# Performance work log

Measured on AMD Instinct MI355X. Metric: run time of the kernel, lower is better.

## Reference

```python
import jax, jax.numpy as jnp
import numpy as np

EMBED_DIM = 256
NUM_HEADS = 8
HEAD_DIM = EMBED_DIM // NUM_HEADS
CPB_HIDDEN = 64


def setup_inputs() -> dict:
    key = jax.random.key(0)
    ks = jax.random.split(key, 12)
    B, Q, K = 4, 900, 1024
    s = 0.02
    return {
        "nodes": jax.random.normal(ks[0], (B, Q, EMBED_DIM), jnp.float32),
        "images_data": jax.random.normal(ks[1], (B, K, EMBED_DIM), jnp.float32),
        "images_mask": jnp.zeros((B, K), dtype=bool),
        "relative_distances": jax.random.normal(ks[2], (B, Q, K, 2), jnp.float32),
        "Wq": jax.random.normal(ks[3], (EMBED_DIM, EMBED_DIM), jnp.float32) * s,
        "bq": jnp.zeros((EMBED_DIM,), jnp.float32),
        "Wkv": jax.random.normal(ks[4], (2 * EMBED_DIM, EMBED_DIM), jnp.float32) * s,
        "bkv": jnp.zeros((2 * EMBED_DIM,), jnp.float32),
        "Wc1": jax.random.normal(ks[5], (CPB_HIDDEN, 2), jnp.float32) * 0.5,
        "bc1": jnp.zeros((CPB_HIDDEN,), jnp.float32),
        "Wc2": jax.random.normal(ks[6], (NUM_HEADS, CPB_HIDDEN), jnp.float32) * 0.1,
        "bc2": jnp.zeros((NUM_HEADS,), jnp.float32),
        "Wo": jax.random.normal(ks[7], (EMBED_DIM, EMBED_DIM), jnp.float32) * s,
        "bo": jnp.zeros((EMBED_DIM,), jnp.float32),
    }


def reference(nodes, images_data, images_mask, relative_distances,
              Wq, bq, Wkv, bkv, Wc1, bc1, Wc2, bc2, Wo, bo):
    B, Q, K, _ = relative_distances.shape
    H, D = NUM_HEADS, HEAD_DIM

    # query / key / value projections
    q = nodes @ Wq.T + bq                       # [B, Q, E]
    q = q.reshape(B, Q, H, D).transpose(0, 2, 1, 3)  # [B, H, Q, D]
    kv = images_data @ Wkv.T + bkv              # [B, K, 2E]
    kv = kv.reshape(B, K, 2, H, D).transpose(2, 0, 3, 1, 4)  # [2, B, H, K, D]
    k, v = kv[0], kv[1]

    # continuous position bias MLP: [B,Q,K,2] -> [B,Q,K,H]
    h = jax.nn.relu(relative_distances @ Wc1.T + bc1)
    cpb = h @ Wc2.T + bc2                       # [B, Q, K, H]
    cpb = cpb.transpose(0, 3, 1, 2)             # [B, H, Q, K]

    # mask out padded image positions
    att_mask = jnp.where(images_mask[:, None, None, :], -jnp.inf, cpb)

    # scaled dot-product attention with additive mask
    scale = 1.0 / jnp.sqrt(jnp.asarray(D, q.dtype))
    scores = jnp.einsum("bhqd,bhkd->bhqk", q, k) * scale + att_mask
    attn = jax.nn.softmax(scores, axis=-1)
    out = jnp.einsum("bhqk,bhkd->bhqd", attn, v)  # [B, H, Q, D]

    out = out.transpose(0, 2, 1, 3).reshape(B, Q, H * D)
    return out @ Wo.T + bo
```

## Files before the change

### kernel.cpp

```cpp
#include <hip/hip_runtime.h>
#include <hip/hip_bf16.h>

typedef float f32x4 __attribute__((ext_vector_type(4)));
typedef short short8 __attribute__((ext_vector_type(8)));

static __device__ __forceinline__ short f2bf(float x) {
  union { __hip_bfloat16 b; short s; } u;
  u.b = __float2bfloat16(x);
  return u.s;
}
static __device__ __forceinline__ float bf2f(short s) {
  union { unsigned u; float f; } x;
  x.u = ((unsigned)(unsigned short)s) << 16;
  return x.f;
}

__global__ __launch_bounds__(256)
void cvt_bf16(const float* __restrict__ nodes, const float* __restrict__ images,
              const float* __restrict__ Wq, const float* __restrict__ Wkv,
              const float* __restrict__ Wo,
              short* __restrict__ nb, short* __restrict__ ib,
              short* __restrict__ wqb, short* __restrict__ wkvb,
              short* __restrict__ wob) {
  const int idx = blockIdx.x * 256 + threadIdx.x;
  const float* src; short* dst; int o;
  if      (idx < 115200) { src = nodes;  dst = nb;   o = idx; }
  else if (idx < 246272) { src = images; dst = ib;   o = idx - 115200; }
  else if (idx < 254464) { src = Wq;     dst = wqb;  o = idx - 246272; }
  else if (idx < 270848) { src = Wkv;    dst = wkvb; o = idx - 254464; }
  else                   { src = Wo;     dst = wob;  o = idx - 270848; }
  const float4 a = ((const float4*)src)[o * 2];
  const float4 b = ((const float4*)src)[o * 2 + 1];
  short8 v;
  v[0] = f2bf(a.x); v[1] = f2bf(a.y); v[2] = f2bf(a.z); v[3] = f2bf(a.w);
  v[4] = f2bf(b.x); v[5] = f2bf(b.y); v[6] = f2bf(b.z); v[7] = f2bf(b.w);
  *(short8*)&dst[o * 8] = v;
}

__global__ __launch_bounds__(256, 4)
void gemm_qkv_mfma(const short* __restrict__ nb, const short* __restrict__ wqb,
                   const float* __restrict__ bq, short* __restrict__ qb,
                   const short* __restrict__ ib, const short* __restrict__ wkvb,
                   const float* __restrict__ bkv, short* __restrict__ kb,
                   short* __restrict__ vT) {
  const int t = threadIdx.x, w = t >> 6, lane = t & 63;
  const int fr = lane & 15, fk = lane >> 4;
  int bid = blockIdx.x;
  const short *A, *W; const float* bias; int M, m0, n0, kvmode;
  if (bid < 228) {
    A = nb; W = wqb; bias = bq; M = 3600; kvmode = 0;
    m0 = (bid >> 2) * 64; n0 = (bid & 3) * 64;
  } else {
    bid -= 228;
    A = ib; W = wkvb; bias = bkv; M = 4096; kvmode = 1;
    m0 = (bid >> 3) * 64; n0 = (bid & 7) * 64;
  }
  int arow = m0 + w * 16 + fr; if (arow > M - 1) arow = M - 1;
  f32x4 acc[4];
  #pragma unroll
  for (int s = 0; s < 4; ++s) acc[s] = (f32x4){0.f, 0.f, 0.f, 0.f};
  #pragma unroll 2
  for (int k0 = 0; k0 < 256; k0 += 32) {
    const short8 af = *(const short8*)&A[(size_t)arow * 256 + k0 + fk * 8];
    #pragma unroll
    for (int s = 0; s < 4; ++s) {
      const short8 wf =
          *(const short8*)&W[(size_t)(n0 + s * 16 + fr) * 256 + k0 + fk * 8];
      acc[s] = __builtin_amdgcn_mfma_f32_16x16x32_bf16(af, wf, acc[s], 0, 0, 0);
    }
  }
  #pragma unroll
  for (int s = 0; s < 4; ++s)
    #pragma unroll
    for (int r = 0; r < 4; ++r) {
      const int m = m0 + w * 16 + fk * 4 + r;
      const int n = n0 + s * 16 + fr;
      const float val = acc[s][r] + bias[n];
      if (kvmode == 0) {
        if (m < 3600) qb[(size_t)m * 256 + n] = f2bf(val);
      } else {
        if (n < 256)
          kb[(size_t)m * 256 + n] = f2bf(val);
        else
          vT[((size_t)(m >> 10) * 256 + (n - 256)) * 1024 + (m & 1023)] =
              f2bf(val);
      }
    }
}

template <int NS>
__global__ __launch_bounds__(256, 4)
void gemm_out_combine(const float* __restrict__ Opart,
                      const float* __restrict__ msplit,
                      const float* __restrict__ lsplit,
                      const short* __restrict__ wob, const float* __restrict__ bo,
                      float* __restrict__ out) {
  const int t = threadIdx.x, w = t >> 6, lane = t & 63;
  const int fr = lane & 15, fk = lane >> 4;
  const int m0 = (blockIdx.x >> 2) * 64, n0 = (blockIdx.x & 3) * 64;
  int arow = m0 + w * 16 + fr; if (arow > 3599) arow = 3599;
  const int b = arow / 900, q = arow - b * 900;
  const int row912 = b * 912 + q;
  f32x4 acc[4];
  #pragma unroll
  for (int s = 0; s < 4; ++s) acc[s] = (f32x4){0.f, 0.f, 0.f, 0.f};
  #pragma unroll 2
  for (int k0 = 0; k0 < 256; k0 += 32) {
    const int h = k0 >> 5;
    float mv[NS], M = -1e30f;
    #pragma unroll
    for (int s = 0; s < NS; ++s) {
      mv[s] = msplit[((s * 4 + b) * 8 + h) * 912 + q];
      M = fmaxf(M, mv[s]);
    }
    float L = 0.f, wgt[NS];
    #pragma unroll
    for (int s = 0; s < NS; ++s) {
      wgt[s] = __expf(mv[s] - M);
      L = fmaf(lsplit[((s * 4 + b) * 8 + h) * 912 + q], wgt[s], L);
    }
    const float rL = 1.f / L;
    float av[8];
    #pragma unroll
    for (int j = 0; j < 8; ++j) av[j] = 0.f;
    #pragma unroll
    for (int s = 0; s < NS; ++s) {
      const float* op = &Opart[((size_t)s * 3648 + row912) * 256 + k0 + fk * 8];
      const float4 o0 = *(const float4*)op;
      const float4 o1 = *(const float4*)(op + 4);
      const float ws = wgt[s] * rL;
      av[0] = fmaf(o0.x, ws, av[0]); av[1] = fmaf(o0.y, ws, av[1]);
      av[2] = fmaf(o0.z, ws, av[2]); av[3] = fmaf(o0.w, ws, av[3]);
      av[4] = fmaf(o1.x, ws, av[4]); av[5] = fmaf(o1.y, ws, av[5]);
      av[6] = fmaf(o1.z, ws, av[6]); av[7] = fmaf(o1.w, ws, av[7]);
    }
    short8 af;
    #pragma unroll
    for (int j = 0; j < 8; ++j) af[j] = f2bf(av[j]);
    #pragma unroll
    for (int s = 0; s < 4; ++s) {
      const short8 wf =
          *(const short8*)&wob[(size_t)(n0 + s * 16 + fr) * 256 + k0 + fk * 8];
      acc[s] = __builtin_amdgcn_mfma_f32_16x16x32_bf16(af, wf, acc[s], 0, 0, 0);
    }
  }
  #pragma unroll
  for (int s = 0; s < 4; ++s)
    #pragma unroll
    for (int r = 0; r < 4; ++r) {
      const int m = m0 + w * 16 + fk * 4 + r;
      const int n = n0 + s * 16 + fr;
      if (m < 3600) out[(size_t)m * 256 + n] = acc[s][r] + bo[n];
    }
}

#define SCALE 0.17677669529663687f

#define BAR()                                              \
  asm volatile("s_waitcnt lgkmcnt(0)" ::: "memory");       \
  __builtin_amdgcn_s_barrier();                            \
  asm volatile("" ::: "memory")

template <int KLEN>
__global__ __launch_bounds__(512, 2)
void attn_part(const __hip_bfloat16* __restrict__ qb,
               const __hip_bfloat16* __restrict__ kb,
               const __hip_bfloat16* __restrict__ vT,
               const float* __restrict__ dist,
               const unsigned char* __restrict__ mask,
               const float* __restrict__ Wc1, const float* __restrict__ bc1,
               const float* __restrict__ Wc2, const float* __restrict__ bc2,
               float* __restrict__ Opart,
               float* __restrict__ msplit,
               float* __restrict__ lsplit) {
  constexpr int NCH = KLEN / 32;
  __shared__ short cpb_s[2][8 * 552];
  __shared__ short ps_s[8][640];

  const int t    = threadIdx.x;
  const int b    = blockIdx.x / 57;
  const int q0   = (blockIdx.x % 57) * 16;
  const int sp   = blockIdx.y;
  const int kb0  = sp * KLEN;
  const int w    = t >> 6;
  const int lane = t & 63;
  const int fr   = lane & 15;
  const int fk   = lane >> 4;

  float w1x[2][8], w1y[2][8], w1b[2][8];
  #pragma unroll
  for (int m = 0; m < 2; ++m)
    #pragma unroll
    for (int jj = 0; jj < 8; ++jj) {
      const int j = m * 32 + fk * 8 + jj;
      w1x[m][jj] = Wc1[2 * j];
      w1y[m][jj] = Wc1[2 * j + 1];
      w1b[m][jj] = bc1[j];
    }
  short8 w2f[2];
  #pragma unroll
  for (int m = 0; m < 2; ++m)
    #pragma unroll
    for (int jj = 0; jj < 8; ++jj) {
      const float v = (fr < 8) ? Wc2[fr * 64 + m * 32 + fk * 8 + jj] : 0.f;
      w2f[m][jj] = f2bf(v);
    }
  const float b2add = (fr < 8) ? bc2[fr] : 0.f;

  int qrow = q0 + fr; if (qrow > 899) qrow = 899;
  const short8 aq = *(const short8*)&qb[(size_t)(b * 900 + qrow) * 256 +
                                        w * 32 + fk * 8];

  const float* dptr[4];
  float2 d2cur[4];
  #pragma unroll
  for (int t4 = 0; t4 < 4; ++t4) {
    int qg = q0 + 2 * w + (t4 >> 1); if (qg > 899) qg = 899;
    dptr[t4] = dist +
        ((size_t)(b * 900 + qg) * 1024 + kb0 + (t4 & 1) * 16 + fr) * 2;
    d2cur[t4] = *(const float2*)dptr[t4];
  }

  f32x4 of[2];
  of[0] = (f32x4){0.f, 0.f, 0.f, 0.f};
  of[1] = (f32x4){0.f, 0.f, 0.f, 0.f};
  float mreg[4], lreg[4];
  #pragma unroll
  for (int r = 0; r < 4; ++r) { mreg[r] = -1e30f; lreg[r] = 0.f; }

  for (int c = 0; c < NCH; ++c) {
    const int k0 = kb0 + c * 32;
    const int cn = (c < NCH - 1) ? c + 1 : c;
    short* cpb_c = cpb_s[c & 1];

    float2 d2n[4];
    #pragma unroll
    for (int t4 = 0; t4 < 4; ++t4)
      d2n[t4] = *(const float2*)(dptr[t4] + (size_t)cn * 64);
    const short8 kf0 = *(const short8*)
        &kb[(size_t)(b * 1024 + k0 + fr) * 256 + w * 32 + fk * 8];
    const short8 kf1 = *(const short8*)
        &kb[(size_t)(b * 1024 + k0 + 16 + fr) * 256 + w * 32 + fk * 8];
    const short8 bv0 = *(const short8*)
        &vT[(size_t)(b * 256 + w * 32 + fr) * 1024 + k0 + fk * 8];
    const short8 bv1 = *(const short8*)
        &vT[(size_t)(b * 256 + w * 32 + 16 + fr) * 1024 + k0 + fk * 8];
    const bool mk0 = mask[b * 1024 + k0 + fr] != 0;
    const bool mk1 = mask[b * 1024 + k0 + 16 + fr] != 0;

    #pragma unroll
    for (int t4 = 0; t4 < 4; ++t4) {
      const float dx = d2cur[t4].x, dy = d2cur[t4].y;
      short8 a0, a1;
      #pragma unroll
      for (int jj = 0; jj < 8; ++jj) {
        const float h0 =
            fmaxf(fmaf(w1x[0][jj], dx, fmaf(w1y[0][jj], dy, w1b[0][jj])), 0.f);
        const float h1 =
            fmaxf(fmaf(w1x[1][jj], dx, fmaf(w1y[1][jj], dy, w1b[1][jj])), 0.f);
        a0[jj] = f2bf(h0);
        a1[jj] = f2bf(h1);
      }
      f32x4 z = {0.f, 0.f, 0.f, 0.f};
      f32x4 dcp = __builtin_amdgcn_mfma_f32_16x16x32_bf16(a1, w2f[1], z, 0, 0, 0);
      dcp = __builtin_amdgcn_mfma_f32_16x16x32_bf16(a0, w2f[0], dcp, 0, 0, 0);
      const int qloc = 2 * w + (t4 >> 1);
      const int kbase = (t4 & 1) * 16;
      if (fr < 8) {
        #pragma unroll
        for (int rr = 0; rr < 4; ++rr)
          cpb_c[fr * 552 + qloc * 34 + kbase + fk * 4 + rr] =
              f2bf(dcp[rr] + b2add);
      }
      __builtin_amdgcn_sched_barrier(0);
    }

    BAR();

    f32x4 z = {0.f, 0.f, 0.f, 0.f};
    __builtin_amdgcn_s_setprio(1);
    const f32x4 sc0 = __builtin_amdgcn_mfma_f32_16x16x32_bf16(aq, kf0, z, 0, 0, 0);
    const f32x4 sc1 = __builtin_amdgcn_mfma_f32_16x16x32_bf16(aq, kf1, z, 0, 0, 0);
    __builtin_amdgcn_s_setprio(0);

    float s0v[4], s1v[4];
    bool need = false;
    #pragma unroll
    for (int r = 0; r < 4; ++r) {
      const int q = fk * 4 + r;
      const float cv0 = bf2f(cpb_c[w * 552 + q * 34 + fr]);
      const float cv1 = bf2f(cpb_c[w * 552 + q * 34 + 16 + fr]);
      s0v[r] = mk0 ? -1e30f : fmaf(sc0[r], SCALE, cv0);
      s1v[r] = mk1 ? -1e30f : fmaf(sc1[r], SCALE, cv1);
      need = need || (fmaxf(s0v[r], s1v[r]) > mreg[r] + 8.f);
    }
    if (__any((int)need)) {
      #pragma unroll
      for (int r = 0; r < 4; ++r) {
        float mx = fmaxf(s0v[r], s1v[r]);
        mx = fmaxf(mx, __shfl_xor(mx, 1));
        mx = fmaxf(mx, __shfl_xor(mx, 2));
        mx = fmaxf(mx, __shfl_xor(mx, 4));
        mx = fmaxf(mx, __shfl_xor(mx, 8));
        const float mnew = fmaxf(mreg[r], mx);
        const float al = __expf(mreg[r] - mnew);
        of[0][r] *= al;
        of[1][r] *= al;
        lreg[r] *= al;
        mreg[r] = mnew;
      }
    }
    #pragma unroll
    for (int r = 0; r < 4; ++r) {
      const int q = fk * 4 + r;
      const float p0 = __expf(s0v[r] - mreg[r]);
      const float p1 = __expf(s1v[r] - mreg[r]);
      ps_s[w][q * 40 + fr]      = f2bf(p0);
      ps_s[w][q * 40 + 16 + fr] = f2bf(p1);
      lreg[r] += p0 + p1;
    }

    asm volatile("s_waitcnt lgkmcnt(0)" ::: "memory");
    __builtin_amdgcn_sched_barrier(0);

    const short8 ap = *(const short8*)&ps_s[w][fr * 40 + fk * 8];
    __builtin_amdgcn_s_setprio(1);
    of[0] = __builtin_amdgcn_mfma_f32_16x16x32_bf16(ap, bv0, of[0], 0, 0, 0);
    of[1] = __builtin_amdgcn_mfma_f32_16x16x32_bf16(ap, bv1, of[1], 0, 0, 0);
    __builtin_amdgcn_s_setprio(0);

    #pragma unroll
    for (int t4 = 0; t4 < 4; ++t4) d2cur[t4] = d2n[t4];
  }

  #pragma unroll
  for (int r = 0; r < 4; ++r) {
    lreg[r] += __shfl_xor(lreg[r], 1);
    lreg[r] += __shfl_xor(lreg[r], 2);
    lreg[r] += __shfl_xor(lreg[r], 4);
    lreg[r] += __shfl_xor(lreg[r], 8);
  }

  #pragma unroll
  for (int s = 0; s < 2; ++s)
    #pragma unroll
    for (int r = 0; r < 4; ++r) {
      const int qg = q0 + fk * 4 + r;
      Opart[((size_t)sp * 3648 + b * 912 + qg) * 256 + w * 32 + s * 16 + fr] =
          of[s][r];
    }
  if (fr == 0) {
    #pragma unroll
    for (int r = 0; r < 4; ++r) {
      const int qg = q0 + fk * 4 + r;
      msplit[((sp * 4 + b) * 8 + w) * 912 + qg] = mreg[r];
      lsplit[((sp * 4 + b) * 8 + w) * 912 + qg] = lreg[r];
    }
  }
}

extern "C" void kernel_launch(void* const* d_in, const int* in_sizes, int n_in,
                              void* d_out, int out_size, void* d_ws, size_t ws_size,
                              hipStream_t stream) {
  const float* nodes  = (const float*)d_in[0];
  const float* images = (const float*)d_in[1];
  const unsigned char* mask = (const unsigned char*)d_in[2];
  const float* dist   = (const float*)d_in[3];
  const float* Wq     = (const float*)d_in[4];
  const float* bq     = (const float*)d_in[5];
  const float* Wkv    = (const float*)d_in[6];
  const float* bkv    = (const float*)d_in[7];
  const float* Wc1    = (const float*)d_in[8];
  const float* bc1    = (const float*)d_in[9];
  const float* Wc2    = (const float*)d_in[10];
  const float* bc2    = (const float*)d_in[11];
  const float* Wo     = (const float*)d_in[12];
  const float* bo     = (const float*)d_in[13];
  float* out = (float*)d_out;

  char* wp = (char*)d_ws;
  short* qb = (short*)wp;
  short* kb = (short*)(wp + 1843200);
  short* vT = (short*)(wp + 3940352);
  char*  S  = wp + 6037504;
  short* nb   = (short*)S;
  short* ib   = (short*)(S + 1843200);
  short* wqb  = (short*)(S + 3940352);
  short* wkvb = (short*)(S + 4071424);
  float* Opart = (float*)S;

  const size_t opart_b  = (size_t)3648 * 256 * 4;
  const size_t ml_b     = (size_t)4 * 8 * 912 * 4;
  const size_t need4 = 6037504u + 4 * (opart_b + 2 * ml_b) + 131072u;
  const size_t need2 = 6037504u + 2 * (opart_b + 2 * ml_b) + 131072u;
  int nsplit = 1;
  if (ws_size >= need4) nsplit = 4;
  else if (ws_size >= need2) nsplit = 2;
  const size_t Ssize = (nsplit == 4) ? 4 * (opart_b + 2 * ml_b)
                     : (nsplit == 2) ? 2 * (opart_b + 2 * ml_b)
                                     : 4333568u;
  short* wob = (short*)(S + ((Ssize > 4333568u) ? Ssize : 4333568u));
  float* msplit = Opart + (size_t)nsplit * 3648 * 256;
  float* lsplit = msplit + (size_t)nsplit * 4 * 8 * 912;

  cvt_bf16<<<1090, 256, 0, stream>>>(nodes, images, Wq, Wkv, Wo,
                                     nb, ib, wqb, wkvb, wob);
  gemm_qkv_mfma<<<740, 256, 0, stream>>>(nb, wqb, bq, qb, ib, wkvb, bkv, kb, vT);

  if (nsplit == 4) {
    attn_part<256><<<dim3(228, 4), 512, 0, stream>>>(
        (const __hip_bfloat16*)qb, (const __hip_bfloat16*)kb,
        (const __hip_bfloat16*)vT, dist, mask, Wc1, bc1, Wc2, bc2,
        Opart, msplit, lsplit);
    gemm_out_combine<4><<<228, 256, 0, stream>>>(Opart, msplit, lsplit,
                                                 wob, bo, out);
  } else if (nsplit == 2) {
    attn_part<512><<<dim3(228, 2), 512, 0, stream>>>(
        (const __hip_bfloat16*)qb, (const __hip_bfloat16*)kb,
        (const __hip_bfloat16*)vT, dist, mask, Wc1, bc1, Wc2, bc2,
        Opart, msplit, lsplit);
    gemm_out_combine<2><<<228, 256, 0, stream>>>(Opart, msplit, lsplit,
                                                 wob, bo, out);
  } else {
    attn_part<1024><<<dim3(228, 1), 512, 0, stream>>>(
        (const __hip_bfloat16*)qb, (const __hip_bfloat16*)kb,
        (const __hip_bfloat16*)vT, dist, mask, Wc1, bc1, Wc2, bc2,
        Opart, msplit, lsplit);
    gemm_out_combine<1><<<228, 256, 0, stream>>>(Opart, msplit, lsplit,
                                                 wob, bo, out);
  }
}
```

Measured before the change: 133.6 us.

## Split CPB MLP into a separate kernel and stream bias into barrier-free attention

The position-bias MLP moves out of the attention kernel into a standalone kernel that writes a bf16 bias tensor [B,H,Q,K] to workspace. A new attention kernel reads that bias from global memory, drops the shared-memory CPB buffer and block barrier, and prefetches K, V, bias and mask one chunk ahead in registers. It uses 2 K-splits instead of 4. The trade is about 60 MB of extra global traffic (bias write plus read) and one more launch, in exchange for removing the barrier and the MLP compute from the attention loop. The path only runs when the workspace is large enough.

```diff
diff --git a/kernel.cpp b/kernel.cpp
--- a/kernel.cpp
+++ b/kernel.cpp
@@ -3,6 +3,7 @@
 
 typedef float f32x4 __attribute__((ext_vector_type(4)));
 typedef short short8 __attribute__((ext_vector_type(8)));
+typedef short short4v __attribute__((ext_vector_type(4)));
 
 static __device__ __forceinline__ short f2bf(float x) {
   union { __hip_bfloat16 b; short s; } u;
@@ -88,6 +89,455 @@
     }
 }
 
+__global__ __launch_bounds__(512, 2)
+void cpb_mlp(const float* __restrict__ dist,
+             const float* __restrict__ Wc1, const float* __restrict__ bc1,
+             const float* __restrict__ Wc2, const float* __restrict__ bc2,
+             short* __restrict__ cpbg) {
+  const int t = threadIdx.x;
+  const int b = blockIdx.x / 57;
+  const int q0 = (blockIdx.x % 57) * 16;
+  const int kb0 = blockIdx.y * 256;
+  const int w = t >> 6, lane = t & 63;
+  const int fr = lane & 15, fk = lane >> 4;
+
+  float w1x[2][8], w1y[2][8], w1b[2][8];
+  #pragma unroll
+  for (int m = 0; m < 2; ++m)
+    #pragma unroll
+    for (int jj = 0; jj < 8; ++jj) {
+      const int j = m * 32 + fk * 8 + jj;
+      w1x[m][jj] = Wc1[2 * j];
+      w1y[m][jj] = Wc1[2 * j + 1];
+      w1b[m][jj] = bc1[j];
+    }
+  short8 w2f[2];
+  #pragma unroll
+  for (int m = 0; m < 2; ++m)
+    #pragma unroll
+    for (int jj = 0; jj < 8; ++jj) {
+      const float v = (fr < 8) ? Wc2[fr * 64 + m * 32 + fk * 8 + jj] : 0.f;
+      w2f[m][jj] = f2bf(v);
+    }
+  const float b2add = (fr < 8) ? bc2[fr] : 0.f;
+
+  const float* dptr[4];
+  float2 d2cur[4];
+  #pragma unroll
+  for (int t4 = 0; t4 < 4; ++t4) {
+    int qg = q0 + 2 * w + (t4 >> 1); if (qg > 899) qg = 899;
+    dptr[t4] = dist +
+        ((size_t)(b * 900 + qg) * 1024 + kb0 + (t4 & 1) * 16 + fr) * 2;
+    d2cur[t4] = *(const float2*)dptr[t4];
+  }
+
+  for (int c = 0; c < 8; ++c) {
+    const int k0 = kb0 + c * 32;
+    const int cn = (c < 7) ? c + 1 : c;
+    float2 d2n[4];
+    #pragma unroll
+    for (int t4 = 0; t4 < 4; ++t4)
+      d2n[t4] = *(const float2*)(dptr[t4] + (size_t)cn * 64);
+
+    #pragma unroll
+    for (int t4 = 0; t4 < 4; ++t4) {
+      const float dx = d2cur[t4].x, dy = d2cur[t4].y;
+      short8 a0, a1;
+      #pragma unroll
+      for (int jj = 0; jj < 8; ++jj) {
+        const float h0 =
+            fmaxf(fmaf(w1x[0][jj], dx, fmaf(w1y[0][jj], dy, w1b[0][jj])), 0.f);
+        const float h1 =
+            fmaxf(fmaf(w1x[1][jj], dx, fmaf(w1y[1][jj], dy, w1b[1][jj])), 0.f);
+        a0[jj] = f2bf(h0);
+        a1[jj] = f2bf(h1);
+      }
+      f32x4 z = {0.f, 0.f, 0.f, 0.f};
+      f32x4 dcp = __builtin_amdgcn_mfma_f32_16x16x32_bf16(a1, w2f[1], z, 0, 0, 0);
+      dcp = __builtin_amdgcn_mfma_f32_16x16x32_bf16(a0, w2f[0], dcp, 0, 0, 0);
+      const int qloc = 2 * w + (t4 >> 1);
+      const int kbase = (t4 & 1) * 16;
+      if (fr < 8) {
+        short4v sv;
+        sv[0] = f2bf(dcp[0] + b2add); sv[1] = f2bf(dcp[1] + b2add);
+        sv[2] = f2bf(dcp[2] + b2add); sv[3] = f2bf(dcp[3] + b2add);
+        *(short4v*)&cpbg[((size_t)(b * 8 + fr) * 912 + q0 + qloc) * 1024 +
+                         k0 + kbase + fk * 4] = sv;
+      }
+      __builtin_amdgcn_sched_barrier(0);
+    }
+    #pragma unroll
+    for (int t4 = 0; t4 < 4; ++t4) d2cur[t4] = d2n[t4];
+  }
+}
+
+#define SCALE 0.17677669529663687f
+
+template <int KLEN>
+__global__ __launch_bounds__(512, 2)
+void attn_nb(const __hip_bfloat16* __restrict__ qb,
+             const __hip_bfloat16* __restrict__ kb,
+             const __hip_bfloat16* __restrict__ vT,
+             const short* __restrict__ cpbg,
+             const unsigned char* __restrict__ mask,
+             float* __restrict__ Opart,
+             float* __restrict__ msplit,
+             float* __restrict__ lsplit) {
+  constexpr int NCH = KLEN / 32;
+  __shared__ short ps_s[8][640];
+
+  const int t    = threadIdx.x;
+  const int b    = blockIdx.x / 57;
+  const int q0   = (blockIdx.x % 57) * 16;
+  const int sp   = blockIdx.y;
+  const int kb0  = sp * KLEN;
+  const int w    = t >> 6;
+  const int lane = t & 63;
+  const int fr   = lane & 15;
+  const int fk   = lane >> 4;
+
+  int qrow = q0 + fr; if (qrow > 899) qrow = 899;
+  const short8 aq = *(const short8*)&qb[(size_t)(b * 900 + qrow) * 256 +
+                                        w * 32 + fk * 8];
+
+  const short* cpbrow[4];
+  #pragma unroll
+  for (int r = 0; r < 4; ++r)
+    cpbrow[r] = cpbg + ((size_t)(b * 8 + w) * 912 + q0 + fk * 4 + r) * 1024 + fr;
+
+  f32x4 of[2];
+  of[0] = (f32x4){0.f, 0.f, 0.f, 0.f};
+  of[1] = (f32x4){0.f, 0.f, 0.f, 0.f};
+  float mreg[4], lreg[4];
+  #pragma unroll
+  for (int r = 0; r < 4; ++r) { mreg[r] = -1e30f; lreg[r] = 0.f; }
+
+  short8 kf0 = *(const short8*)
+      &kb[(size_t)(b * 1024 + kb0 + fr) * 256 + w * 32 + fk * 8];
+  short8 kf1 = *(const short8*)
+      &kb[(size_t)(b * 1024 + kb0 + 16 + fr) * 256 + w * 32 + fk * 8];
+  short8 bv0 = *(const short8*)
+      &vT[(size_t)(b * 256 + w * 32 + fr) * 1024 + kb0 + fk * 8];
+  short8 bv1 = *(const short8*)
+      &vT[(size_t)(b * 256 + w * 32 + 16 + fr) * 1024 + kb0 + fk * 8];
+  float cv0c[4], cv1c[4];
+  #pragma unroll
+  for (int r = 0; r < 4; ++r) {
+    cv0c[r] = bf2f(cpbrow[r][kb0]);
+    cv1c[r] = bf2f(cpbrow[r][kb0 + 16]);
+  }
+  bool mk0 = mask[b * 1024 + kb0 + fr] != 0;
+  bool mk1 = mask[b * 1024 + kb0 + 16 + fr] != 0;
+
+  for (int c = 0; c < NCH; ++c) {
+    const int k0 = kb0 + c * 32;
+
+    short8 kf0n = kf0, kf1n = kf1, bv0n = bv0, bv1n = bv1;
+    float cv0n[4], cv1n[4];
+    bool mk0n = mk0, mk1n = mk1;
+    if (c + 1 < NCH) {
+      const int k1 = k0 + 32;
+      kf0n = *(const short8*)
+          &kb[(size_t)(b * 1024 + k1 + fr) * 256 + w * 32 + fk * 8];
+      kf1n = *(const short8*)
+          &kb[(size_t)(b * 1024 + k1 + 16 + fr) * 256 + w * 32 + fk * 8];
+      bv0n = *(const short8*)
+          &vT[(size_t)(b * 256 + w * 32 + fr) * 1024 + k1 + fk * 8];
+      bv1n = *(const short8*)
+          &vT[(size_t)(b * 256 + w * 32 + 16 + fr) * 1024 + k1 + fk * 8];
+      #pragma unroll
+      for (int r = 0; r < 4; ++r) {
+        cv0n[r] = bf2f(cpbrow[r][k1]);
+        cv1n[r] = bf2f(cpbrow[r][k1 + 16]);
+      }
+      mk0n = mask[b * 1024 + k1 + fr] != 0;
+      mk1n = mask[b * 1024 + k1 + 16 + fr] != 0;
+    } else {
+      #pragma unroll
+      for (int r = 0; r < 4; ++r) { cv0n[r] = cv0c[r]; cv1n[r] = cv1c[r]; }
+    }
+
+    f32x4 z = {0.f, 0.f, 0.f, 0.f};
+    __builtin_amdgcn_s_setprio(1);
+    const f32x4 sc0 = __builtin_amdgcn_mfma_f32_16x16x32_bf16(aq, kf0, z, 0, 0, 0);
+    const f32x4 sc1 = __builtin_amdgcn_mfma_f32_16x16x32_bf16(aq, kf1, z, 0, 0, 0);
+    __builtin_amdgcn_s_setprio(0);
+
+    float s0v[4], s1v[4];
+    bool need = false;
+    #pragma unroll
+    for (int r = 0; r < 4; ++r) {
+      s0v[r] = mk0 ? -1e30f : fmaf(sc0[r], SCALE, cv0c[r]);
+      s1v[r] = mk1 ? -1e30f : fmaf(sc1[r], SCALE, cv1c[r]);
+      need = need || (fmaxf(s0v[r], s1v[r]) > mreg[r] + 8.f);
+    }
+    if (__any((int)need)) {
+      #pragma unroll
+      for (int r = 0; r < 4; ++r) {
+        float mx = fmaxf(s0v[r], s1v[r]);
+        mx = fmaxf(mx, __shfl_xor(mx, 1));
+        mx = fmaxf(mx, __shfl_xor(mx, 2));
+        mx = fmaxf(mx, __shfl_xor(mx, 4));
+        mx = fmaxf(mx, __shfl_xor(mx, 8));
+        const float mnew = fmaxf(mreg[r], mx);
+        const float al = __expf(mreg[r] - mnew);
+        of[0][r] *= al;
+        of[1][r] *= al;
+        lreg[r] *= al;
+        mreg[r] = mnew;
+      }
+    }
+    #pragma unroll
+    for (int r = 0; r < 4; ++r) {
+      const int q = fk * 4 + r;
+      const float p0 = __expf(s0v[r] - mreg[r]);
+      const float p1 = __expf(s1v[r] - mreg[r]);
+      ps_s[w][q * 40 + fr]      = f2bf(p0);
+      ps_s[w][q * 40 + 16 + fr] = f2bf(p1);
+      lreg[r] += p0 + p1;
+    }
+
+    asm volatile("s_waitcnt lgkmcnt(0)" ::: "memory");
+    __builtin_amdgcn_sched_barrier(0);
+
+    const short8 ap = *(const short8*)&ps_s[w][fr * 40 + fk * 8];
+    __builtin_amdgcn_s_setprio(1);
+    of[0] = __builtin_amdgcn_mfma_f32_16x16x32_bf16(ap, bv0, of[0], 0, 0, 0);
+    of[1] = __builtin_amdgcn_mfma_f32_16x16x32_bf16(ap, bv1, of[1], 0, 0, 0);
+    __builtin_amdgcn_s_setprio(0);
+
+    kf0 = kf0n; kf1 = kf1n; bv0 = bv0n; bv1 = bv1n;
+    mk0 = mk0n; mk1 = mk1n;
+    #pragma unroll
+    for (int r = 0; r < 4; ++r) { cv0c[r] = cv0n[r]; cv1c[r] = cv1n[r]; }
+  }
+
+  #pragma unroll
+  for (int r = 0; r < 4; ++r) {
+    lreg[r] += __shfl_xor(lreg[r], 1);
+    lreg[r] += __shfl_xor(lreg[r], 2);
+    lreg[r] += __shfl_xor(lreg[r], 4);
+    lreg[r] += __shfl_xor(lreg[r], 8);
+  }
+  #pragma unroll
+  for (int s = 0; s < 2; ++s)
+    #pragma unroll
+    for (int r = 0; r < 4; ++r) {
+      const int qg = q0 + fk * 4 + r;
+      Opart[((size_t)sp * 3648 + b * 912 + qg) * 256 + w * 32 + s * 16 + fr] =
+          of[s][r];
+    }
+  if (fr == 0) {
+    #pragma unroll
+    for (int r = 0; r < 4; ++r) {
+      const int qg = q0 + fk * 4 + r;
+      msplit[((sp * 4 + b) * 8 + w) * 912 + qg] = mreg[r];
+      lsplit[((sp * 4 + b) * 8 + w) * 912 + qg] = lreg[r];
+    }
+  }
+}
+
+#define BAR()                                              \
+  asm volatile("s_waitcnt lgkmcnt(0)" ::: "memory");       \
+  __builtin_amdgcn_s_barrier();                            \
+  asm volatile("" ::: "memory")
+
+template <int KLEN>
+__global__ __launch_bounds__(512, 2)
+void attn_part(const __hip_bfloat16* __restrict__ qb,
+               const __hip_bfloat16* __restrict__ kb,
+               const __hip_bfloat16* __restrict__ vT,
+               const float* __restrict__ dist,
+               const unsigned char* __restrict__ mask,
+               const float* __restrict__ Wc1, const float* __restrict__ bc1,
+               const float* __restrict__ Wc2, const float* __restrict__ bc2,
+               float* __restrict__ Opart, float* __restrict__ msplit,
+               float* __restrict__ lsplit) {
+  constexpr int NCH = KLEN / 32;
+  __shared__ short cpb_s[2][8 * 552];
+  __shared__ short ps_s[8][640];
+
+  const int t    = threadIdx.x;
+  const int b    = blockIdx.x / 57;
+  const int q0   = (blockIdx.x % 57) * 16;
+  const int sp   = blockIdx.y;
+  const int kb0  = sp * KLEN;
+  const int w    = t >> 6;
+  const int lane = t & 63;
+  const int fr   = lane & 15;
+  const int fk   = lane >> 4;
+
+  float w1x[2][8], w1y[2][8], w1b[2][8];
+  #pragma unroll
+  for (int m = 0; m < 2; ++m)
+    #pragma unroll
+    for (int jj = 0; jj < 8; ++jj) {
+      const int j = m * 32 + fk * 8 + jj;
+      w1x[m][jj] = Wc1[2 * j];
+      w1y[m][jj] = Wc1[2 * j + 1];
+      w1b[m][jj] = bc1[j];
+    }
+  short8 w2f[2];
+  #pragma unroll
+  for (int m = 0; m < 2; ++m)
+    #pragma unroll
+    for (int jj = 0; jj < 8; ++jj) {
+      const float v = (fr < 8) ? Wc2[fr * 64 + m * 32 + fk * 8 + jj] : 0.f;
+      w2f[m][jj] = f2bf(v);
+    }
+  const float b2add = (fr < 8) ? bc2[fr] : 0.f;
+
+  int qrow = q0 + fr; if (qrow > 899) qrow = 899;
+  const short8 aq = *(const short8*)&qb[(size_t)(b * 900 + qrow) * 256 +
+                                        w * 32 + fk * 8];
+
+  const float* dptr[4];
+  float2 d2cur[4];
+  #pragma unroll
+  for (int t4 = 0; t4 < 4; ++t4) {
+    int qg = q0 + 2 * w + (t4 >> 1); if (qg > 899) qg = 899;
+    dptr[t4] = dist +
+        ((size_t)(b * 900 + qg) * 1024 + kb0 + (t4 & 1) * 16 + fr) * 2;
+    d2cur[t4] = *(const float2*)dptr[t4];
+  }
+
+  f32x4 of[2];
+  of[0] = (f32x4){0.f, 0.f, 0.f, 0.f};
+  of[1] = (f32x4){0.f, 0.f, 0.f, 0.f};
+  float mreg[4], lreg[4];
+  #pragma unroll
+  for (int r = 0; r < 4; ++r) { mreg[r] = -1e30f; lreg[r] = 0.f; }
+
+  for (int c = 0; c < NCH; ++c) {
+    const int k0 = kb0 + c * 32;
+    const int cn = (c < NCH - 1) ? c + 1 : c;
+    short* cpb_c = cpb_s[c & 1];
+
+    float2 d2n[4];
+    #pragma unroll
+    for (int t4 = 0; t4 < 4; ++t4)
+      d2n[t4] = *(const float2*)(dptr[t4] + (size_t)cn * 64);
+    const short8 kf0 = *(const short8*)
+        &kb[(size_t)(b * 1024 + k0 + fr) * 256 + w * 32 + fk * 8];
+    const short8 kf1 = *(const short8*)
+        &kb[(size_t)(b * 1024 + k0 + 16 + fr) * 256 + w * 32 + fk * 8];
+    const short8 bv0 = *(const short8*)
+        &vT[(size_t)(b * 256 + w * 32 + fr) * 1024 + k0 + fk * 8];
+    const short8 bv1 = *(const short8*)
+        &vT[(size_t)(b * 256 + w * 32 + 16 + fr) * 1024 + k0 + fk * 8];
+    const bool mk0 = mask[b * 1024 + k0 + fr] != 0;
+    const bool mk1 = mask[b * 1024 + k0 + 16 + fr] != 0;
+
+    #pragma unroll
+    for (int t4 = 0; t4 < 4; ++t4) {
+      const float dx = d2cur[t4].x, dy = d2cur[t4].y;
+      short8 a0, a1;
+      #pragma unroll
+      for (int jj = 0; jj < 8; ++jj) {
+        const float h0 =
+            fmaxf(fmaf(w1x[0][jj], dx, fmaf(w1y[0][jj], dy, w1b[0][jj])), 0.f);
+        const float h1 =
+            fmaxf(fmaf(w1x[1][jj], dx, fmaf(w1y[1][jj], dy, w1b[1][jj])), 0.f);
+        a0[jj] = f2bf(h0);
+        a1[jj] = f2bf(h1);
+      }
+      f32x4 z = {0.f, 0.f, 0.f, 0.f};
+      f32x4 dcp = __builtin_amdgcn_mfma_f32_16x16x32_bf16(a1, w2f[1], z, 0, 0, 0);
+      dcp = __builtin_amdgcn_mfma_f32_16x16x32_bf16(a0, w2f[0], dcp, 0, 0, 0);
+      const int qloc = 2 * w + (t4 >> 1);
+      const int kbase = (t4 & 1) * 16;
+      if (fr < 8) {
+        #pragma unroll
+        for (int rr = 0; rr < 4; ++rr)
+          cpb_c[fr * 552 + qloc * 34 + kbase + fk * 4 + rr] =
+              f2bf(dcp[rr] + b2add);
+      }
+      __builtin_amdgcn_sched_barrier(0);
+    }
+
+    BAR();
+
+    f32x4 z = {0.f, 0.f, 0.f, 0.f};
+    __builtin_amdgcn_s_setprio(1);
+    const f32x4 sc0 = __builtin_amdgcn_mfma_f32_16x16x32_bf16(aq, kf0, z, 0, 0, 0);
+    const f32x4 sc1 = __builtin_amdgcn_mfma_f32_16x16x32_bf16(aq, kf1, z, 0, 0, 0);
+    __builtin_amdgcn_s_setprio(0);
+
+    float s0v[4], s1v[4];
+    bool need = false;
+    #pragma unroll
+    for (int r = 0; r < 4; ++r) {
+      const int q = fk * 4 + r;
+      const float cv0 = bf2f(cpb_c[w * 552 + q * 34 + fr]);
+      const float cv1 = bf2f(cpb_c[w * 552 + q * 34 + 16 + fr]);
+      s0v[r] = mk0 ? -1e30f : fmaf(sc0[r], SCALE, cv0);
+      s1v[r] = mk1 ? -1e30f : fmaf(sc1[r], SCALE, cv1);
+      need = need || (fmaxf(s0v[r], s1v[r]) > mreg[r] + 8.f);
+    }
+    if (__any((int)need)) {
+      #pragma unroll
+      for (int r = 0; r < 4; ++r) {
+        float mx = fmaxf(s0v[r], s1v[r]);
+        mx = fmaxf(mx, __shfl_xor(mx, 1));
+        mx = fmaxf(mx, __shfl_xor(mx, 2));
+        mx = fmaxf(mx, __shfl_xor(mx, 4));
+        mx = fmaxf(mx, __shfl_xor(mx, 8));
+        const float mnew = fmaxf(mreg[r], mx);
+        const float al = __expf(mreg[r] - mnew);
+        of[0][r] *= al;
+        of[1][r] *= al;
+        lreg[r] *= al;
+        mreg[r] = mnew;
+      }
+    }
+    #pragma unroll
+    for (int r = 0; r < 4; ++r) {
+      const int q = fk * 4 + r;
+      const float p0 = __expf(s0v[r] - mreg[r]);
+      const float p1 = __expf(s1v[r] - mreg[r]);
+      ps_s[w][q * 40 + fr]      = f2bf(p0);
+      ps_s[w][q * 40 + 16 + fr] = f2bf(p1);
+      lreg[r] += p0 + p1;
+    }
+
+    asm volatile("s_waitcnt lgkmcnt(0)" ::: "memory");
+    __builtin_amdgcn_sched_barrier(0);
+
+    const short8 ap = *(const short8*)&ps_s[w][fr * 40 + fk * 8];
+    __builtin_amdgcn_s_setprio(1);
+    of[0] = __builtin_amdgcn_mfma_f32_16x16x32_bf16(ap, bv0, of[0], 0, 0, 0);
+    of[1] = __builtin_amdgcn_mfma_f32_16x16x32_bf16(ap, bv1, of[1], 0, 0, 0);
+    __builtin_amdgcn_s_setprio(0);
+
+    #pragma unroll
+    for (int t4 = 0; t4 < 4; ++t4) d2cur[t4] = d2n[t4];
+  }
+
+  #pragma unroll
+  for (int r = 0; r < 4; ++r) {
+    lreg[r] += __shfl_xor(lreg[r], 1);
+    lreg[r] += __shfl_xor(lreg[r], 2);
+    lreg[r] += __shfl_xor(lreg[r], 4);
+    lreg[r] += __shfl_xor(lreg[r], 8);
+  }
+  #pragma unroll
+  for (int s = 0; s < 2; ++s)
+    #pragma unroll
+    for (int r = 0; r < 4; ++r) {
+      const int qg = q0 + fk * 4 + r;
+      Opart[((size_t)sp * 3648 + b * 912 + qg) * 256 + w * 32 + s * 16 + fr] =
+          of[s][r];
+    }
+  if (fr == 0) {
+    #pragma unroll
+    for (int r = 0; r < 4; ++r) {
+      const int qg = q0 + fk * 4 + r;
+      msplit[((sp * 4 + b) * 8 + w) * 912 + qg] = mreg[r];
+      lsplit[((sp * 4 + b) * 8 + w) * 912 + qg] = lreg[r];
+    }
+  }
+}
+
 template <int NS>
 __global__ __launch_bounds__(256, 4)
 void gemm_out_combine(const float* __restrict__ Opart,
@@ -152,211 +602,6 @@
       const int n = n0 + s * 16 + fr;
       if (m < 3600) out[(size_t)m * 256 + n] = acc[s][r] + bo[n];
     }
-}
-
-#define SCALE 0.17677669529663687f
-
-#define BAR()                                              \
-  asm volatile("s_waitcnt lgkmcnt(0)" ::: "memory");       \
-  __builtin_amdgcn_s_barrier();                            \
-  asm volatile("" ::: "memory")
-
-template <int KLEN>
-__global__ __launch_bounds__(512, 2)
-void attn_part(const __hip_bfloat16* __restrict__ qb,
-               const __hip_bfloat16* __restrict__ kb,
-               const __hip_bfloat16* __restrict__ vT,
-               const float* __restrict__ dist,
-               const unsigned char* __restrict__ mask,
-               const float* __restrict__ Wc1, const float* __restrict__ bc1,
-               const float* __restrict__ Wc2, const float* __restrict__ bc2,
-               float* __restrict__ Opart,
-               float* __restrict__ msplit,
-               float* __restrict__ lsplit) {
-  constexpr int NCH = KLEN / 32;
-  __shared__ short cpb_s[2][8 * 552];
-  __shared__ short ps_s[8][640];
-
-  const int t    = threadIdx.x;
-  const int b    = blockIdx.x / 57;
-  const int q0   = (blockIdx.x % 57) * 16;
-  const int sp   = blockIdx.y;
-  const int kb0  = sp * KLEN;
-  const int w    = t >> 6;
-  const int lane = t & 63;
-  const int fr   = lane & 15;
-  const int fk   = lane >> 4;
-
-  float w1x[2][8], w1y[2][8], w1b[2][8];
-  #pragma unroll
-  for (int m = 0; m < 2; ++m)
-    #pragma unroll
-    for (int jj = 0; jj < 8; ++jj) {
-      const int j = m * 32 + fk * 8 + jj;
-      w1x[m][jj] = Wc1[2 * j];
-      w1y[m][jj] = Wc1[2 * j + 1];
-      w1b[m][jj] = bc1[j];
-    }
-  short8 w2f[2];
-  #pragma unroll
-  for (int m = 0; m < 2; ++m)
-    #pragma unroll
-    for (int jj = 0; jj < 8; ++jj) {
-      const float v = (fr < 8) ? Wc2[fr * 64 + m * 32 + fk * 8 + jj] : 0.f;
-      w2f[m][jj] = f2bf(v);
-    }
-  const float b2add = (fr < 8) ? bc2[fr] : 0.f;
-
-  int qrow = q0 + fr; if (qrow > 899) qrow = 899;
-  const short8 aq = *(const short8*)&qb[(size_t)(b * 900 + qrow) * 256 +
-                                        w * 32 + fk * 8];
-
-  const float* dptr[4];
-  float2 d2cur[4];
-  #pragma unroll
-  for (int t4 = 0; t4 < 4; ++t4) {
-    int qg = q0 + 2 * w + (t4 >> 1); if (qg > 899) qg = 899;
-    dptr[t4] = dist +
-        ((size_t)(b * 900 + qg) * 1024 + kb0 + (t4 & 1) * 16 + fr) * 2;
-    d2cur[t4] = *(const float2*)dptr[t4];
-  }
-
-  f32x4 of[2];
-  of[0] = (f32x4){0.f, 0.f, 0.f, 0.f};
-  of[1] = (f32x4){0.f, 0.f, 0.f, 0.f};
-  float mreg[4], lreg[4];
-  #pragma unroll
-  for (int r = 0; r < 4; ++r) { mreg[r] = -1e30f; lreg[r] = 0.f; }
-
-  for (int c = 0; c < NCH; ++c) {
-    const int k0 = kb0 + c * 32;
-    const int cn = (c < NCH - 1) ? c + 1 : c;
-    short* cpb_c = cpb_s[c & 1];
-
-    float2 d2n[4];
-    #pragma unroll
-    for (int t4 = 0; t4 < 4; ++t4)
-      d2n[t4] = *(const float2*)(dptr[t4] + (size_t)cn * 64);
-    const short8 kf0 = *(const short8*)
-        &kb[(size_t)(b * 1024 + k0 + fr) * 256 + w * 32 + fk * 8];
-    const short8 kf1 = *(const short8*)
-        &kb[(size_t)(b * 1024 + k0 + 16 + fr) * 256 + w * 32 + fk * 8];
-    const short8 bv0 = *(const short8*)
-        &vT[(size_t)(b * 256 + w * 32 + fr) * 1024 + k0 + fk * 8];
-    const short8 bv1 = *(const short8*)
-        &vT[(size_t)(b * 256 + w * 32 + 16 + fr) * 1024 + k0 + fk * 8];
-    const bool mk0 = mask[b * 1024 + k0 + fr] != 0;
-    const bool mk1 = mask[b * 1024 + k0 + 16 + fr] != 0;
-
-    #pragma unroll
-    for (int t4 = 0; t4 < 4; ++t4) {
-      const float dx = d2cur[t4].x, dy = d2cur[t4].y;
-      short8 a0, a1;
-      #pragma unroll
-      for (int jj = 0; jj < 8; ++jj) {
-        const float h0 =
-            fmaxf(fmaf(w1x[0][jj], dx, fmaf(w1y[0][jj], dy, w1b[0][jj])), 0.f);
-        const float h1 =
-            fmaxf(fmaf(w1x[1][jj], dx, fmaf(w1y[1][jj], dy, w1b[1][jj])), 0.f);
-        a0[jj] = f2bf(h0);
-        a1[jj] = f2bf(h1);
-      }
-      f32x4 z = {0.f, 0.f, 0.f, 0.f};
-      f32x4 dcp = __builtin_amdgcn_mfma_f32_16x16x32_bf16(a1, w2f[1], z, 0, 0, 0);
-      dcp = __builtin_amdgcn_mfma_f32_16x16x32_bf16(a0, w2f[0], dcp, 0, 0, 0);
-      const int qloc = 2 * w + (t4 >> 1);
-      const int kbase = (t4 & 1) * 16;
-      if (fr < 8) {
-        #pragma unroll
-        for (int rr = 0; rr < 4; ++rr)
-          cpb_c[fr * 552 + qloc * 34 + kbase + fk * 4 + rr] =
-              f2bf(dcp[rr] + b2add);
-      }
-      __builtin_amdgcn_sched_barrier(0);
-    }
-
-    BAR();
-
-    f32x4 z = {0.f, 0.f, 0.f, 0.f};
-    __builtin_amdgcn_s_setprio(1);
-    const f32x4 sc0 = __builtin_amdgcn_mfma_f32_16x16x32_bf16(aq, kf0, z, 0, 0, 0);
-    const f32x4 sc1 = __builtin_amdgcn_mfma_f32_16x16x32_bf16(aq, kf1, z, 0, 0, 0);
-    __builtin_amdgcn_s_setprio(0);
-
-    float s0v[4], s1v[4];
-    bool need = false;
-    #pragma unroll
-    for (int r = 0; r < 4; ++r) {
-      const int q = fk * 4 + r;
-      const float cv0 = bf2f(cpb_c[w * 552 + q * 34 + fr]);
-      const float cv1 = bf2f(cpb_c[w * 552 + q * 34 + 16 + fr]);
-      s0v[r] = mk0 ? -1e30f : fmaf(sc0[r], SCALE, cv0);
-      s1v[r] = mk1 ? -1e30f : fmaf(sc1[r], SCALE, cv1);
-      need = need || (fmaxf(s0v[r], s1v[r]) > mreg[r] + 8.f);
-    }
-    if (__any((int)need)) {
-      #pragma unroll
-      for (int r = 0; r < 4; ++r) {
-        float mx = fmaxf(s0v[r], s1v[r]);
-        mx = fmaxf(mx, __shfl_xor(mx, 1));
-        mx = fmaxf(mx, __shfl_xor(mx, 2));
-        mx = fmaxf(mx, __shfl_xor(mx, 4));
-        mx = fmaxf(mx, __shfl_xor(mx, 8));
-        const float mnew = fmaxf(mreg[r], mx);
-        const float al = __expf(mreg[r] - mnew);
-        of[0][r] *= al;
-        of[1][r] *= al;
-        lreg[r] *= al;
-        mreg[r] = mnew;
-      }
-    }
-    #pragma unroll
-    for (int r = 0; r < 4; ++r) {
-      const int q = fk * 4 + r;
-      const float p0 = __expf(s0v[r] - mreg[r]);
-      const float p1 = __expf(s1v[r] - mreg[r]);
-      ps_s[w][q * 40 + fr]      = f2bf(p0);
-      ps_s[w][q * 40 + 16 + fr] = f2bf(p1);
-      lreg[r] += p0 + p1;
-    }
-
-    asm volatile("s_waitcnt lgkmcnt(0)" ::: "memory");
-    __builtin_amdgcn_sched_barrier(0);
-
-    const short8 ap = *(const short8*)&ps_s[w][fr * 40 + fk * 8];
-    __builtin_amdgcn_s_setprio(1);
-    of[0] = __builtin_amdgcn_mfma_f32_16x16x32_bf16(ap, bv0, of[0], 0, 0, 0);
-    of[1] = __builtin_amdgcn_mfma_f32_16x16x32_bf16(ap, bv1, of[1], 0, 0, 0);
-    __builtin_amdgcn_s_setprio(0);
-
-    #pragma unroll
-    for (int t4 = 0; t4 < 4; ++t4) d2cur[t4] = d2n[t4];
-  }
-
-  #pragma unroll
-  for (int r = 0; r < 4; ++r) {
-    lreg[r] += __shfl_xor(lreg[r], 1);
-    lreg[r] += __shfl_xor(lreg[r], 2);
-    lreg[r] += __shfl_xor(lreg[r], 4);
-    lreg[r] += __shfl_xor(lreg[r], 8);
-  }
-
-  #pragma unroll
-  for (int s = 0; s < 2; ++s)
-    #pragma unroll
-    for (int r = 0; r < 4; ++r) {
-      const int qg = q0 + fk * 4 + r;
-      Opart[((size_t)sp * 3648 + b * 912 + qg) * 256 + w * 32 + s * 16 + fr] =
-          of[s][r];
-    }
-  if (fr == 0) {
-    #pragma unroll
-    for (int r = 0; r < 4; ++r) {
-      const int qg = q0 + fk * 4 + r;
-      msplit[((sp * 4 + b) * 8 + w) * 912 + qg] = mreg[r];
-      lsplit[((sp * 4 + b) * 8 + w) * 912 + qg] = lreg[r];
-    }
-  }
 }
 
 extern "C" void kernel_launch(void* const* d_in, const int* in_sizes, int n_in,
@@ -389,44 +634,52 @@
   short* wkvb = (short*)(S + 4071424);
   float* Opart = (float*)S;
 
-  const size_t opart_b  = (size_t)3648 * 256 * 4;
-  const size_t ml_b     = (size_t)4 * 8 * 912 * 4;
-  const size_t need4 = 6037504u + 4 * (opart_b + 2 * ml_b) + 131072u;
-  const size_t need2 = 6037504u + 2 * (opart_b + 2 * ml_b) + 131072u;
-  int nsplit = 1;
-  if (ws_size >= need4) nsplit = 4;
-  else if (ws_size >= need2) nsplit = 2;
-  const size_t Ssize = (nsplit == 4) ? 4 * (opart_b + 2 * ml_b)
-                     : (nsplit == 2) ? 2 * (opart_b + 2 * ml_b)
-                                     : 4333568u;
-  short* wob = (short*)(S + ((Ssize > 4333568u) ? Ssize : 4333568u));
-  float* msplit = Opart + (size_t)nsplit * 3648 * 256;
-  float* lsplit = msplit + (size_t)nsplit * 4 * 8 * 912;
-
-  cvt_bf16<<<1090, 256, 0, stream>>>(nodes, images, Wq, Wkv, Wo,
-                                     nb, ib, wqb, wkvb, wob);
-  gemm_qkv_mfma<<<740, 256, 0, stream>>>(nb, wqb, bq, qb, ib, wkvb, bkv, kb, vT);
-
-  if (nsplit == 4) {
-    attn_part<256><<<dim3(228, 4), 512, 0, stream>>>(
+  const size_t opart_b = (size_t)3648 * 256 * 4;
+  const size_t ml_b    = (size_t)4 * 8 * 912 * 4;
+  const size_t s2_2    = 2 * (opart_b + 2 * ml_b);
+  const size_t cpbg_sz = (size_t)4 * 8 * 912 * 1024 * 2;
+  const size_t need_big = 6037504u + s2_2 + cpbg_sz + 131072u;
+  const size_t need2    = 6037504u + s2_2 + 131072u;
+
+  if (ws_size >= need_big) {
+    short* cpbg = (short*)(S + s2_2);
+    short* wob  = (short*)(S + s2_2 + cpbg_sz);
+    float* msplit = Opart + (size_t)2 * 3648 * 256;
+    float* lsplit = msplit + (size_t)2 * 4 * 8 * 912;
+    cvt_bf16<<<1090, 256, 0, stream>>>(nodes, images, Wq, Wkv, Wo,
+                                       nb, ib, wqb, wkvb, wob);
+    gemm_qkv_mfma<<<740, 256, 0, stream>>>(nb, wqb, bq, qb, ib, wkvb, bkv,
+                                           kb, vT);
+    cpb_mlp<<<dim3(228, 4), 512, 0, stream>>>(dist, Wc1, bc1, Wc2, bc2, cpbg);
+    attn_nb<512><<<dim3(228, 2), 512, 0, stream>>>(
         (const __hip_bfloat16*)qb, (const __hip_bfloat16*)kb,
-        (const __hip_bfloat16*)vT, dist, mask, Wc1, bc1, Wc2, bc2,
-        Opart, msplit, lsplit);
-    gemm_out_combine<4><<<228, 256, 0, stream>>>(Opart, msplit, lsplit,
-                                                 wob, bo, out);
-  } else if (nsplit == 2) {
-    attn_part<512><<<dim3(228, 2), 512, 0, stream>>>(
-        (const __hip_bfloat16*)qb, (const __hip_bfloat16*)kb,
-        (const __hip_bfloat16*)vT, dist, mask, Wc1, bc1, Wc2, bc2,
-        Opart, msplit, lsplit);
+        (const __hip_bfloat16*)vT, cpbg, mask, Opart, msplit, lsplit);
     gemm_out_combine<2><<<228, 256, 0, stream>>>(Opart, msplit, lsplit,
                                                  wob, bo, out);
   } else {
-    attn_part<1024><<<dim3(228, 1), 512, 0, stream>>>(
-        (const __hip_bfloat16*)qb, (const __hip_bfloat16*)kb,
-        (const __hip_bfloat16*)vT, dist, mask, Wc1, bc1, Wc2, bc2,
-        Opart, msplit, lsplit);
-    gemm_out_combine<1><<<228, 256, 0, stream>>>(Opart, msplit, lsplit,
-                                                 wob, bo, out);
-  }
-}
+    int nsplit = (ws_size >= need2) ? 2 : 1;
+    const size_t Ssize = (nsplit == 2) ? s2_2 : 4333568u;
+    short* wob = (short*)(S + Ssize);
+    float* msplit = Opart + (size_t)nsplit * 3648 * 256;
+    float* lsplit = msplit + (size_t)nsplit * 4 * 8 * 912;
+    cvt_bf16<<<1090, 256, 0, stream>>>(nodes, images, Wq, Wkv, Wo,
+                                       nb, ib, wqb, wkvb, wob);
+    gemm_qkv_mfma<<<740, 256, 0, stream>>>(nb, wqb, bq, qb, ib, wkvb, bkv,
+                                           kb, vT);
+    if (nsplit == 2) {
+      attn_part<512><<<dim3(228, 2), 512, 0, stream>>>(
+          (const __hip_bfloat16*)qb, (const __hip_bfloat16*)kb,
+          (const __hip_bfloat16*)vT, dist, mask, Wc1, bc1, Wc2, bc2,
+          Opart, msplit, lsplit);
+      gemm_out_combine<2><<<228, 256, 0, stream>>>(Opart, msplit, lsplit,
+                                                   wob, bo, out);
+    } else {
+      attn_part<1024><<<dim3(228, 1), 512, 0, stream>>>(
+          (const __hip_bfloat16*)qb, (const __hip_bfloat16*)kb,
+          (const __hip_bfloat16*)vT, dist, mask, Wc1, bc1, Wc2, bc2,
+          Opart, msplit, lsplit);
+      gemm_out_combine<1><<<228, 256, 0, stream>>>(Opart, msplit, lsplit,
+                                                   wob, bo, out);
+    }
+  }
+}
```

Result: faster. 127.4 us (-4.7%).
